# Kernel optimization log

Measured on AMD Instinct MI355X. Metric: run time of the kernel, lower is better.

## Reference

```python
import jax, jax.numpy as jnp
import numpy as np
from jax import lax

KSIZE = 11      # torchmetrics SSIM default gaussian kernel size
SIGMA = 1.5     # torchmetrics default sigma
K1, K2 = 0.01, 0.03
DATA_RANGE = 1.0
BLOCK = 8


def _gaussian2d():
    coords = jnp.arange(KSIZE, dtype=jnp.float32) - (KSIZE - 1) / 2.0
    g = jnp.exp(-(coords ** 2) / (2.0 * SIGMA ** 2))
    g = g / g.sum()
    return jnp.outer(g, g)  # (K, K)


def _blockify(x, block):
    # (B, C, H, W) -> (B*nby*nbx, C, block, block)
    B, C, H, W = x.shape
    x = x.reshape(B, C, H // block, block, W // block, block)
    x = x.transpose(0, 2, 4, 1, 3, 5)
    return x.reshape(-1, C, block, block)


def _blockwise_ssim_mean(x, y):
    # x, y: (N, C, BLOCK, BLOCK). Returns mean SSIM over all blocks/pixels.
    N, C = x.shape[0], x.shape[1]
    pad = (KSIZE - 1) // 2
    pw = ((0, 0), (0, 0), (pad, pad), (pad, pad))
    xp = jnp.pad(x, pw, mode='reflect')
    yp = jnp.pad(y, pw, mode='reflect')
    # stack [x, y, x*x, y*y, x*y] along channels -> single depthwise conv
    stats = jnp.concatenate([xp, yp, xp * xp, yp * yp, xp * yp], axis=1)
    kern = jnp.broadcast_to(_gaussian2d()[None, None], (5 * C, 1, KSIZE, KSIZE)).astype(x.dtype)
    out = lax.conv_general_dilated(
        stats, kern, window_strides=(1, 1), padding='VALID',
        dimension_numbers=('NCHW', 'OIHW', 'NCHW'), feature_group_count=5 * C)
    mu_x, mu_y = out[:, 0:C], out[:, C:2 * C]
    mu_xx, mu_yy, mu_xy = out[:, 2 * C:3 * C], out[:, 3 * C:4 * C], out[:, 4 * C:5 * C]
    sigma_x = mu_xx - mu_x * mu_x
    sigma_y = mu_yy - mu_y * mu_y
    sigma_xy = mu_xy - mu_x * mu_y
    c1 = (K1 * DATA_RANGE) ** 2
    c2 = (K2 * DATA_RANGE) ** 2
    ssim_map = ((2.0 * mu_x * mu_y + c1) * (2.0 * sigma_xy + c2)) / (
        (mu_x * mu_x + mu_y * mu_y + c1) * (sigma_x + sigma_y + c2))
    return ssim_map.mean()


def setup_inputs() -> dict:
    key = jax.random.key(0)
    k1, k2 = jax.random.split(key)
    shape = (16, 3, 512, 512)
    inputs = jax.random.uniform(k1, shape, dtype=jnp.float32)
    targets = jax.random.uniform(k2, shape, dtype=jnp.float32)
    return {"inputs": inputs, "targets": targets}


def reference(inputs, targets):
    # Original loops over 8x8 blocks calling SSIM per block and averages
    # (1 - ssim_block). All blocks have identical pixel counts, so this
    # equals 1 - mean(ssim over all blocks), computed in one fused pass.
    xb = _blockify(inputs, BLOCK)   # y_true blocks
    yb = _blockify(targets, BLOCK)  # y_pred blocks (SSIM is symmetric)
    return 1.0 - _blockwise_ssim_mean(yb, xb)
```

## Files before the change

### kernel.cpp

```cpp
#include <hip/hip_runtime.h>
#include <math.h>


#define NBC     196608
#define NPIX    12582912.0
#define GRID1   6144
#define PAD     12
#define GSTRIDE 100
#define FIXSCALE 1073741824.0f
#define C1      1.0e-4f
#define C2      9.0e-4f

struct WMat { float w[64]; };

__device__ __forceinline__ void matvec8(const float* __restrict__ w,
                                        const float S[8], float O[8]) {
#pragma unroll
    for (int i = 0; i < 8; i++) {
        float a = w[i * 8 + 0] * S[0];
#pragma unroll
        for (int c = 1; c < 8; c++) a = fmaf(w[i * 8 + c], S[c], a);
        O[i] = a;
    }
}

__device__ __forceinline__ void twrite(float* tile, int l, const float A[8]) {
    float4* d = reinterpret_cast<float4*>(tile + l * PAD);
    d[0] = make_float4(A[0], A[1], A[2], A[3]);
    d[1] = make_float4(A[4], A[5], A[6], A[7]);
}

__device__ __forceinline__ void tread(const float* tile, int l, float A[8]) {
#pragma unroll
    for (int c = 0; c < 8; c++) A[c] = tile[c * PAD + l];
}

__global__ __launch_bounds__(256) void ssim_partial(const float* __restrict__ x,
                                                    const float* __restrict__ y,
                                                    unsigned long long* __restrict__ acc64,
                                                    WMat Wm) {
    __shared__ __align__(16) float lds[2 * 32 * GSTRIDE];
    __shared__ float redbuf[4];

    const int tid = threadIdx.x;
    const int l   = tid & 7;
    const int grp = tid >> 3;
    const int bc  = blockIdx.x * 32 + grp;

    const int wb  = bc & 63;
    const int hb  = (bc >> 6) & 63;
    const int img = bc >> 12;

    const int rowbase = (img * 512 + hb * 8 + l) * 512 + wb * 8;

    const float4 x0 = *reinterpret_cast<const float4*>(x + rowbase);
    const float4 x1 = *reinterpret_cast<const float4*>(x + rowbase + 4);
    const float4 y0 = *reinterpret_cast<const float4*>(y + rowbase);
    const float4 y1 = *reinterpret_cast<const float4*>(y + rowbase + 4);

    float X[8] = {x0.x, x0.y, x0.z, x0.w, x1.x, x1.y, x1.z, x1.w};
    float Y[8] = {y0.x, y0.y, y0.z, y0.w, y1.x, y1.y, y1.z, y1.w};

    const float* w = Wm.w;
    float* t0 = &lds[grp * GSTRIDE];
    float* t1 = &lds[32 * GSTRIDE + grp * GSTRIDE];

    float A[8], Ccol[8], T[8];
    float mx[8], my[8], mxx[8], myy[8], mxy[8];

    matvec8(w, X, A);  twrite(t0, l, A);
    __syncthreads();
    tread(t0, l, Ccol); matvec8(w, Ccol, mx);
    matvec8(w, Y, A);  twrite(t1, l, A);
    __syncthreads();
    tread(t1, l, Ccol); matvec8(w, Ccol, my);
#pragma unroll
    for (int i = 0; i < 8; i++) T[i] = X[i] * X[i];
    matvec8(w, T, A);  twrite(t0, l, A);
    __syncthreads();
    tread(t0, l, Ccol); matvec8(w, Ccol, mxx);
#pragma unroll
    for (int i = 0; i < 8; i++) T[i] = Y[i] * Y[i];
    matvec8(w, T, A);  twrite(t1, l, A);
    __syncthreads();
    tread(t1, l, Ccol); matvec8(w, Ccol, myy);
#pragma unroll
    for (int i = 0; i < 8; i++) T[i] = X[i] * Y[i];
    matvec8(w, T, A);  twrite(t0, l, A);
    __syncthreads();
    tread(t0, l, Ccol); matvec8(w, Ccol, mxy);

    float s = 0.f;
#pragma unroll
    for (int p = 0; p < 8; p++) {
        float a = mx[p], b = my[p];
        float sx  = mxx[p] - a * a;
        float sy  = myy[p] - b * b;
        float sxy = mxy[p] - a * b;
        float num = fmaf(2.f, a * b, C1) * fmaf(2.f, sxy, C2);
        float den = (fmaf(a, a, b * b) + C1) * (sx + sy + C2);
        float r = __builtin_amdgcn_rcpf(den);
        r = r * (2.f - den * r);
        s = fmaf(num, r, s);
    }

#pragma unroll
    for (int off = 32; off > 0; off >>= 1) s += __shfl_xor(s, off, 64);
    if ((tid & 63) == 0) redbuf[tid >> 6] = s;
    __syncthreads();
    if (tid == 0) {
        float bs = (redbuf[0] + redbuf[1]) + (redbuf[2] + redbuf[3]);
        long long fx = llrintf(bs * FIXSCALE);
        atomicAdd(acc64, (unsigned long long)fx);
    }
}

__global__ void zero_acc(unsigned long long* p) { *p = 0ull; }

__global__ void ssim_final(const unsigned long long* __restrict__ acc64,
                           float* __restrict__ out) {
    long long s = (long long)*acc64;
    out[0] = (float)(1.0 - ((double)s / (double)FIXSCALE) / NPIX);
}

static WMat make_w() {
    double g[11]; double s = 0.0;
    for (int k = 0; k < 11; k++) { double d = k - 5.0; g[k] = exp(-d * d / 4.5); s += g[k]; }
    for (int k = 0; k < 11; k++) g[k] /= s;
    WMat W{};
    for (int j = 0; j < 8; j++)
        for (int k = 0; k < 11; k++) {
            int t = j + k - 5;
            int rr = t < 0 ? -t : (t > 7 ? 14 - t : t);
            W.w[j * 8 + rr] += (float)g[k];
        }
    return W;
}

extern "C" void kernel_launch(void* const* d_in, const int* in_sizes, int n_in,
                              void* d_out, int out_size, void* d_ws, size_t ws_size,
                              hipStream_t stream) {
    const float* x = (const float*)d_in[0];
    const float* y = (const float*)d_in[1];
    unsigned long long* acc64 = (unsigned long long*)d_ws;
    WMat W = make_w();
    zero_acc<<<1, 1, 0, stream>>>(acc64);
    ssim_partial<<<GRID1, 256, 0, stream>>>(x, y, acc64, W);
    ssim_final<<<1, 1, 0, stream>>>(acc64, (float*)d_out);
}
```

Measured before the change: 176.1 us.

## Transpose via ds_swizzle, spread atomics over slots, fuse finalization into last block

Replaces the LDS tile transpose and its per-stage barriers with an in-register butterfly transpose using ds_swizzle across each 8-lane group. The global accumulation now goes to 16 slots instead of one, which reduces atomic contention. The last block to finish, detected with a counter, computes the final result, which removes the separate finalize kernel; the zero kernel becomes a memset. The swizzle adds select and swap instructions and raises register pressure, and occupancy is hinted at 4 blocks per unit.

```diff
diff --git a/kernel.cpp b/kernel.cpp
--- a/kernel.cpp
+++ b/kernel.cpp
@@ -2,16 +2,36 @@
 #include <math.h>
 
 
-#define NBC     196608
-#define NPIX    12582912.0
-#define GRID1   6144
-#define PAD     12
-#define GSTRIDE 100
+#define NBC      196608
+#define NPIX     12582912.0
+#define GRID1    6144
+#define NSLOT    16
 #define FIXSCALE 1073741824.0f
-#define C1      1.0e-4f
-#define C2      9.0e-4f
+#define C1       1.0e-4f
+#define C2       9.0e-4f
 
 struct WMat { float w[64]; };
+
+template<int OFF>
+__device__ __forceinline__ float swzf(float v) {
+    return __int_as_float(__builtin_amdgcn_ds_swizzle(__float_as_int(v), OFF));
+}
+
+#define BPAIR(p, q, OFFC) do {                  \
+        float t = b ? A[p] : A[q];              \
+        float r = swzf<OFFC>(t);                \
+        A[p] = b ? r : A[p];                    \
+        A[q] = b ? A[q] : r;                    \
+    } while (0)
+
+__device__ __forceinline__ void transpose8(float A[8], int l) {
+    { const bool b = (l & 1) != 0;
+      BPAIR(0,1,0x041F); BPAIR(2,3,0x041F); BPAIR(4,5,0x041F); BPAIR(6,7,0x041F); }
+    { const bool b = (l & 2) != 0;
+      BPAIR(0,2,0x081F); BPAIR(1,3,0x081F); BPAIR(4,6,0x081F); BPAIR(5,7,0x081F); }
+    { const bool b = (l & 4) != 0;
+      BPAIR(0,4,0x101F); BPAIR(1,5,0x101F); BPAIR(2,6,0x101F); BPAIR(3,7,0x101F); }
+}
 
 __device__ __forceinline__ void matvec8(const float* __restrict__ w,
                                         const float S[8], float O[8]) {
@@ -24,22 +44,20 @@
     }
 }
 
-__device__ __forceinline__ void twrite(float* tile, int l, const float A[8]) {
-    float4* d = reinterpret_cast<float4*>(tile + l * PAD);
-    d[0] = make_float4(A[0], A[1], A[2], A[3]);
-    d[1] = make_float4(A[4], A[5], A[6], A[7]);
+__device__ __forceinline__ void sandwich(const float* __restrict__ w,
+                                         const float S[8], float out_v[8], int l) {
+    float A[8];
+    matvec8(w, S, A);
+    transpose8(A, l);
+    matvec8(w, A, out_v);
 }
 
-__device__ __forceinline__ void tread(const float* tile, int l, float A[8]) {
-#pragma unroll
-    for (int c = 0; c < 8; c++) A[c] = tile[c * PAD + l];
-}
-
-__global__ __launch_bounds__(256) void ssim_partial(const float* __restrict__ x,
-                                                    const float* __restrict__ y,
-                                                    unsigned long long* __restrict__ acc64,
-                                                    WMat Wm) {
-    __shared__ __align__(16) float lds[2 * 32 * GSTRIDE];
+__global__ __launch_bounds__(256, 4) void ssim_fused(const float* __restrict__ x,
+                                                     const float* __restrict__ y,
+                                                     unsigned long long* __restrict__ slots,
+                                                     unsigned* __restrict__ counter,
+                                                     float* __restrict__ out,
+                                                     WMat Wm) {
     __shared__ float redbuf[4];
 
     const int tid = threadIdx.x;
@@ -62,33 +80,19 @@
     float Y[8] = {y0.x, y0.y, y0.z, y0.w, y1.x, y1.y, y1.z, y1.w};
 
     const float* w = Wm.w;
-    float* t0 = &lds[grp * GSTRIDE];
-    float* t1 = &lds[32 * GSTRIDE + grp * GSTRIDE];
 
-    float A[8], Ccol[8], T[8];
-    float mx[8], my[8], mxx[8], myy[8], mxy[8];
-
-    matvec8(w, X, A);  twrite(t0, l, A);
-    __syncthreads();
-    tread(t0, l, Ccol); matvec8(w, Ccol, mx);
-    matvec8(w, Y, A);  twrite(t1, l, A);
-    __syncthreads();
-    tread(t1, l, Ccol); matvec8(w, Ccol, my);
+    float mx[8], my[8], mxx[8], myy[8], mxy[8], T[8];
+    sandwich(w, X, mx, l);
+    sandwich(w, Y, my, l);
 #pragma unroll
     for (int i = 0; i < 8; i++) T[i] = X[i] * X[i];
-    matvec8(w, T, A);  twrite(t0, l, A);
-    __syncthreads();
-    tread(t0, l, Ccol); matvec8(w, Ccol, mxx);
+    sandwich(w, T, mxx, l);
 #pragma unroll
     for (int i = 0; i < 8; i++) T[i] = Y[i] * Y[i];
-    matvec8(w, T, A);  twrite(t1, l, A);
-    __syncthreads();
-    tread(t1, l, Ccol); matvec8(w, Ccol, myy);
+    sandwich(w, T, myy, l);
 #pragma unroll
     for (int i = 0; i < 8; i++) T[i] = X[i] * Y[i];
-    matvec8(w, T, A);  twrite(t0, l, A);
-    __syncthreads();
-    tread(t0, l, Ccol); matvec8(w, Ccol, mxy);
+    sandwich(w, T, mxy, l);
 
     float s = 0.f;
 #pragma unroll
@@ -111,16 +115,18 @@
     if (tid == 0) {
         float bs = (redbuf[0] + redbuf[1]) + (redbuf[2] + redbuf[3]);
         long long fx = llrintf(bs * FIXSCALE);
-        atomicAdd(acc64, (unsigned long long)fx);
+        atomicAdd(&slots[blockIdx.x & (NSLOT - 1)], (unsigned long long)fx);
+        __threadfence();
+        unsigned old = atomicAdd(counter, 1u);
+        if (old == (unsigned)(GRID1 - 1)) {
+            __threadfence();
+            long long tot = 0;
+#pragma unroll
+            for (int i = 0; i < NSLOT; i++)
+                tot += (long long)atomicAdd(&slots[i], 0ull);
+            out[0] = (float)(1.0 - ((double)tot / (double)FIXSCALE) / NPIX);
+        }
     }
-}
-
-__global__ void zero_acc(unsigned long long* p) { *p = 0ull; }
-
-__global__ void ssim_final(const unsigned long long* __restrict__ acc64,
-                           float* __restrict__ out) {
-    long long s = (long long)*acc64;
-    out[0] = (float)(1.0 - ((double)s / (double)FIXSCALE) / NPIX);
 }
 
 static WMat make_w() {
@@ -142,9 +148,9 @@
                               hipStream_t stream) {
     const float* x = (const float*)d_in[0];
     const float* y = (const float*)d_in[1];
-    unsigned long long* acc64 = (unsigned long long*)d_ws;
+    unsigned long long* slots = (unsigned long long*)d_ws;
+    unsigned* counter = (unsigned*)((char*)d_ws + NSLOT * 8);
     WMat W = make_w();
-    zero_acc<<<1, 1, 0, stream>>>(acc64);
-    ssim_partial<<<GRID1, 256, 0, stream>>>(x, y, acc64, W);
-    ssim_final<<<1, 1, 0, stream>>>(acc64, (float*)d_out);
+    hipMemsetAsync(d_ws, 0, NSLOT * 8 + 4, stream);
+    ssim_fused<<<GRID1, 256, 0, stream>>>(x, y, slots, counter, (float*)d_out, W);
 }
```

Result: slower. 362.1 us (+105.6%).
